# Performance work log

Hardware: AMD Instinct MI355X
Metric: run time of the kernel (lower is better)

## Reference

```python
import jax, jax.numpy as jnp
import numpy as np

B, S, V, D = 4, 128, 50257, 1024

def setup_inputs() -> dict:
    key = jax.random.key(0)
    k1, k2 = jax.random.split(key)
    # pred_probs: a probability simplex over vocab per (b, s); module initializes
    # to uniform by default, we use normalized uniform noise for a non-degenerate test.
    p = jax.random.uniform(k1, (B, S, V), dtype=jnp.float32) + 1e-3
    pred_probs = p / jnp.sum(p, axis=-1, keepdims=True)
    embed_weight = jax.random.normal(k2, (V, D), dtype=jnp.float32) * 0.02
    return {"pred_probs": pred_probs, "embed_weight": embed_weight}

def reference(pred_probs, embed_weight):
    # do_sample=False, st=False default path of TargetProbability.forward_multiple
    # predictions: argmax over vocab
    predictions = jnp.argmax(pred_probs, axis=-1)  # [B, S] int
    # soft embedding: (pred_probs.unsqueeze(-1) * embed_lut.weight).sum(-2)
    # == GEMM over the vocab dim, avoiding the [B,S,V,D] intermediate.
    pred_emb = jnp.einsum('bsv,vd->bsd', pred_probs, embed_weight)  # [B, S, D]
    return pred_emb, predictions, pred_probs
```

## Files before the change

kernel.cpp:

```cpp
#include <hip/hip_runtime.h>

#define MROWS 512
#define VDIM  50257
#define KP    50304
#define NDIM  1024
#define NST32 1572
#define KSPLIT 32
#define SC     25
#define PRED_OFF 524288
#define PP_OFF   524800
#define NPREP  4096
#define CHUNK  6288
#define NCONVW 12576

typedef unsigned short u16;
typedef unsigned int   u32;
typedef unsigned long long u64;
typedef __bf16 bf16x8 __attribute__((ext_vector_type(8)));
typedef u16    u16x8  __attribute__((ext_vector_type(8)));
typedef float  f32x4  __attribute__((ext_vector_type(4)));
typedef float  f32x4u __attribute__((ext_vector_type(4), aligned(4)));

__device__ __forceinline__ u16 f2bf(float f) {
  u32 u = __float_as_uint(f);
  u32 r = (u + 0x7fffu + ((u >> 16) & 1u)) >> 16;
  return (u16)r;
}

__device__ __forceinline__ void gl_lds16(const u16* g, u16* l) {
  __builtin_amdgcn_global_load_lds(
      (const __attribute__((address_space(1))) u32*)(g),
      (__attribute__((address_space(3))) u32*)(l), 16, 0, 0);
}

__global__ __launch_bounds__(256) void prep_fused(const float* __restrict__ P,
                                                  const float* __restrict__ W,
                                                  float* __restrict__ out,
                                                  u16* __restrict__ A,
                                                  u16* __restrict__ BT,
                                                  u64* __restrict__ amax)
{
  const int tid = threadIdx.x;
  const int bx  = blockIdx.x;
  if (bx < NPREP) {
    const int m  = bx >> 3;
    const int c  = bx & 7;
    const int s0 = c * CHUNK;
    const int len = min(VDIM - s0, CHUNK);
    const float* row = P + (size_t)m * VDIM;
    float*       crw = out + PP_OFF + (size_t)m * VDIM;
    u16*        arow = A + (size_t)m * KP;

    if (tid < 32) { f32x4 z = {}; *(f32x4*)(out + (size_t)m * NDIM + c * 128 + tid * 4) = z; }

    u64 best = 0;
#define TRK(val, idx) do { \
      u64 pk = ((u64)__float_as_uint(val) << 32) | (u64)(0xFFFFu - (u32)(idx)); \
      best = best > pk ? best : pk; } while (0)
#define GRP(cc) do {                                                     \
      f32x4u va = *(const f32x4u*)(row + (cc));                          \
      f32x4u vb = *(const f32x4u*)(row + (cc) + 4);                      \
      *(f32x4u*)(crw + (cc))     = va;                                   \
      *(f32x4u*)(crw + (cc) + 4) = vb;                                   \
      u16x8 o;                                                           \
      o[0]=f2bf(va[0]); o[1]=f2bf(va[1]); o[2]=f2bf(va[2]); o[3]=f2bf(va[3]); \
      o[4]=f2bf(vb[0]); o[5]=f2bf(vb[1]); o[6]=f2bf(vb[2]); o[7]=f2bf(vb[3]); \
      *(u16x8*)(arow + (cc)) = o;                                        \
      TRK(va[0],(cc)); TRK(va[1],(cc)+1); TRK(va[2],(cc)+2); TRK(va[3],(cc)+3); \
      TRK(vb[0],(cc)+4); TRK(vb[1],(cc)+5); TRK(vb[2],(cc)+6); TRK(vb[3],(cc)+7); \
    } while (0)

    const int ng = len >> 3;
    int i = tid;
    for (; i + 256 < ng; i += 512) {
      const int c0 = s0 + (i << 3);
      const int c1 = c0 + 2048;
      GRP(c0);
      GRP(c1);
    }
    if (i < ng) GRP(s0 + (i << 3));
    if (tid < (len & 7)) {
      const int col = s0 + (ng << 3) + tid;
      float v = row[col];
      crw[col] = v;
      arow[col] = f2bf(v);
      TRK(v, col);
    }
#undef GRP
#undef TRK
    if (c == 7 && tid < KP - VDIM) arow[VDIM + tid] = 0;

    __shared__ u64 sb[256];
    sb[tid] = best;
    __syncthreads();
    for (int s = 128; s > 0; s >>= 1) {
      if (tid < s) { u64 o = sb[tid + s]; if (o > sb[tid]) sb[tid] = o; }
      __syncthreads();
    }
    if (tid == 0) atomicMax(&amax[m], sb[0]);
  } else {
    const int cidx = bx - NPREP;
    __shared__ u16 t[64][65];
    const int dt  = cidx & 15;
    const int vt  = cidx >> 4;
    const int v0  = vt << 6;
    const int d0  = dt << 6;
    const int c16 = tid & 15;
    const int r16 = tid >> 4;
#pragma unroll
    for (int p = 0; p < 4; ++p) {
      const int v  = v0 + p * 16 + r16;
      const int vl = p * 16 + r16;
      float4 w = make_float4(0.f, 0.f, 0.f, 0.f);
      if (v < VDIM) w = *(const float4*)(W + (size_t)v * NDIM + d0 + c16 * 4);
      t[c16 * 4 + 0][vl] = f2bf(w.x);
      t[c16 * 4 + 1][vl] = f2bf(w.y);
      t[c16 * 4 + 2][vl] = f2bf(w.z);
      t[c16 * 4 + 3][vl] = f2bf(w.w);
    }
    __syncthreads();
#pragma unroll
    for (int p = 0; p < 4; ++p) {
      const int dl = p * 16 + r16;
      const int vl = c16 * 4;
      ushort4 o;
      o.x = t[dl][vl]; o.y = t[dl][vl + 1]; o.z = t[dl][vl + 2]; o.w = t[dl][vl + 3];
      *(ushort4*)(BT + (size_t)(d0 + dl) * KP + v0 + vl) = o;
    }
  }
}

__global__ __launch_bounds__(512, 1) void gemm_kernel(const u16* __restrict__ A,
                                                      const u16* __restrict__ BT,
                                                      const u64* __restrict__ amax,
                                                      float* __restrict__ out)
{
  __shared__ u16 ldsA[4][256 * 32];
  __shared__ u16 ldsB[4][256 * 32];

  const int bx  = blockIdx.x;
  const int kc  = (bx & 7) | ((bx >> 6) << 3);
  const int mn  = (bx >> 3) & 7;
  const int m0  = (mn & 1) << 8;
  const int n0  = (mn >> 1) << 8;
  const int ks0 = kc * SC * 2;
  const int ks1 = min(NST32, ks0 + SC * 2);
  const int tid  = threadIdx.x;
  const int wid  = tid >> 6;
  const int lane = tid & 63;
  const int wr   = wid >> 2;
  const int wc   = wid & 3;

  if (bx == 0) {
    u64 p = amax[tid];
    out[PRED_OFF + tid] = (float)(0xFFFF - (int)(p & 0xFFFFu));
  }

  const int sp  = lane >> 3;
  const int sx  = (lane & 7) ^ sp;
  const int srow = 2 * sp + (sx >> 2);
  const int skel = (sx & 3) << 3;
  const u16* gA = A  + (size_t)(m0 + wid * 32 + srow) * KP + skel;
  const u16* gB = BT + (size_t)(n0 + wid * 32 + srow) * KP + skel;

  f32x4 acc[8][4] = {};

  const int r   = lane & 15;
  const int q4  = lane >> 4;
  const int sl  = (((r & 1) << 2) | q4) ^ ((r >> 1) & 7);
  const int rb2A = (wr * 128 + (r & ~1)) * 32 + sl * 8;
  const int rb2B = (wc * 64  + (r & ~1)) * 32 + sl * 8;

#define STAGE_A(buf, ks) do {                                            \
    const size_t k_ = (size_t)(ks) << 5;                                 \
    gl_lds16(gA + k_,                 &ldsA[buf][(wid * 32) * 32]);      \
    gl_lds16(gA + k_ + (size_t)16*KP, &ldsA[buf][(wid * 32 + 16) * 32]); \
  } while (0)
#define STAGE_B(buf, ks) do {                                            \
    const size_t k_ = (size_t)(ks) << 5;                                 \
    gl_lds16(gB + k_,                 &ldsB[buf][(wid * 32) * 32]);      \
    gl_lds16(gB + k_ + (size_t)16*KP, &ldsB[buf][(wid * 32 + 16) * 32]); \
  } while (0)

  STAGE_A(0, ks0); STAGE_B(0, ks0);
  if (ks0 + 1 < ks1) { STAGE_A(1, ks0 + 1); STAGE_B(1, ks0 + 1); }
  if (ks0 + 2 < ks1) { STAGE_A(2, ks0 + 2); STAGE_B(2, ks0 + 2); }
  if (ks0 + 2 < ks1)      asm volatile("s_waitcnt vmcnt(8)" ::: "memory");
  else if (ks0 + 1 < ks1) asm volatile("s_waitcnt vmcnt(4)" ::: "memory");
  else                    asm volatile("s_waitcnt vmcnt(0)" ::: "memory");
  __builtin_amdgcn_s_barrier();

  int b = 0;
  for (int ks = ks0; ks < ks1; ++ks) {
    const u16* lA = ldsA[b];
    const u16* lB = ldsB[b];

    bf16x8 av[4], bv[4];
#pragma unroll
    for (int i = 0; i < 4; ++i) av[i] = *(const bf16x8*)(lA + rb2A + i * 512);
#pragma unroll
    for (int j = 0; j < 4; ++j) bv[j] = *(const bf16x8*)(lB + rb2B + j * 512);
    if (ks + 3 < ks1) STAGE_A((b + 3) & 3, ks + 3);
    __builtin_amdgcn_s_barrier();
    asm volatile("s_waitcnt lgkmcnt(0)" ::: "memory");
    __builtin_amdgcn_sched_barrier(0);
    __builtin_amdgcn_s_setprio(1);
#pragma unroll
    for (int i = 0; i < 4; ++i)
#pragma unroll
      for (int j = 0; j < 4; ++j)
        acc[i][j] = __builtin_amdgcn_mfma_f32_16x16x32_bf16(av[i], bv[j], acc[i][j], 0, 0, 0);
    __builtin_amdgcn_s_setprio(0);
    __builtin_amdgcn_s_barrier();

    bf16x8 aw[4];
#pragma unroll
    for (int i = 0; i < 4; ++i) aw[i] = *(const bf16x8*)(lA + rb2A + (i + 4) * 512);
    if (ks + 3 < ks1) STAGE_B((b + 3) & 3, ks + 3);
    __builtin_amdgcn_s_barrier();
    asm volatile("s_waitcnt lgkmcnt(0)" ::: "memory");
    __builtin_amdgcn_sched_barrier(0);
    __builtin_amdgcn_s_setprio(1);
#pragma unroll
    for (int i = 0; i < 4; ++i)
#pragma unroll
      for (int j = 0; j < 4; ++j)
        acc[i + 4][j] = __builtin_amdgcn_mfma_f32_16x16x32_bf16(aw[i], bv[j], acc[i + 4][j], 0, 0, 0);
    __builtin_amdgcn_s_setprio(0);
    if (ks + 3 < ks1)      asm volatile("s_waitcnt vmcnt(8)" ::: "memory");
    else if (ks + 2 < ks1) asm volatile("s_waitcnt vmcnt(4)" ::: "memory");
    else if (ks + 1 < ks1) asm volatile("s_waitcnt vmcnt(0)" ::: "memory");
    __builtin_amdgcn_s_barrier();
    b = (b + 1) & 3;
  }
#undef STAGE_A
#undef STAGE_B

  const int col = lane & 15;
  const int r4  = q4 << 2;
#pragma unroll
  for (int i = 0; i < 8; ++i)
#pragma unroll
    for (int j = 0; j < 4; ++j)
#pragma unroll
      for (int rr = 0; rr < 4; ++rr) {
        const int mm = m0 + wr * 128 + i * 16 + r4 + rr;
        const int nn = n0 + wc * 64 + j * 16 + col;
        atomicAdd(out + (size_t)mm * NDIM + nn, acc[i][j][rr]);
      }
}

extern "C" void kernel_launch(void* const* d_in, const int* in_sizes, int n_in,
                              void* d_out, int out_size, void* d_ws, size_t ws_size,
                              hipStream_t stream) {
  const float* P = (const float*)d_in[0];
  const float* W = (const float*)d_in[1];
  float* out = (float*)d_out;
  u64* amax = (u64*)d_ws;
  u16* A  = (u16*)((char*)d_ws + 4096);
  u16* BT = A + (size_t)MROWS * KP;

  hipMemsetAsync(amax, 0, MROWS * sizeof(u64), stream);
  prep_fused<<<NPREP + NCONVW, 256, 0, stream>>>(P, W, out, A, BT, amax);
  gemm_kernel<<<256, 512, 0, stream>>>(A, BT, amax, out);
}
```

Before: 223.6 us.

## Split prep kernel, double split-K, and switch GEMM to 2-stage double buffering

Splits the fused prep kernel into separate P-conversion/argmax and W-transpose kernels, and doubles the GEMM split-K from 32 to 64 chunks, launching 512 blocks with launch bounds allowing 2 blocks per CU. The GEMM pipeline drops from a 4-deep LDS ring with interleaved half-steps to a simpler 2-deep double buffer, which halves LDS so two workgroups can be co-resident. The intent is more parallelism and occupancy across the machine. In exchange, prefetch depth shrinks, there are twice as many atomic adds into the output, and there is one extra kernel launch.

```diff
diff --git a/kernel.cpp b/kernel.cpp
--- a/kernel.cpp
+++ b/kernel.cpp
@@ -5,8 +5,7 @@
 #define KP    50304
 #define NDIM  1024
 #define NST32 1572
-#define KSPLIT 32
-#define SC     25
+#define KSPLIT 64
 #define PRED_OFF 524288
 #define PP_OFF   524800
 #define NPREP  4096
@@ -33,118 +32,119 @@
       (__attribute__((address_space(3))) u32*)(l), 16, 0, 0);
 }
 
-__global__ __launch_bounds__(256) void prep_fused(const float* __restrict__ P,
-                                                  const float* __restrict__ W,
-                                                  float* __restrict__ out,
-                                                  u16* __restrict__ A,
-                                                  u16* __restrict__ BT,
-                                                  u64* __restrict__ amax)
+__global__ __launch_bounds__(256) void prep_kernel(const float* __restrict__ P,
+                                                   float* __restrict__ out,
+                                                   u16* __restrict__ A,
+                                                   u64* __restrict__ amax)
 {
   const int tid = threadIdx.x;
   const int bx  = blockIdx.x;
-  if (bx < NPREP) {
-    const int m  = bx >> 3;
-    const int c  = bx & 7;
-    const int s0 = c * CHUNK;
-    const int len = min(VDIM - s0, CHUNK);
-    const float* row = P + (size_t)m * VDIM;
-    float*       crw = out + PP_OFF + (size_t)m * VDIM;
-    u16*        arow = A + (size_t)m * KP;
-
-    if (tid < 32) { f32x4 z = {}; *(f32x4*)(out + (size_t)m * NDIM + c * 128 + tid * 4) = z; }
-
-    u64 best = 0;
+  const int m  = bx >> 3;
+  const int c  = bx & 7;
+  const int s0 = c * CHUNK;
+  const int len = min(VDIM - s0, CHUNK);
+  const float* row = P + (size_t)m * VDIM;
+  float*       crw = out + PP_OFF + (size_t)m * VDIM;
+  u16*        arow = A + (size_t)m * KP;
+
+  if (tid < 32) { f32x4 z = {}; *(f32x4*)(out + (size_t)m * NDIM + c * 128 + tid * 4) = z; }
+
+  u64 best = 0;
 #define TRK(val, idx) do { \
-      u64 pk = ((u64)__float_as_uint(val) << 32) | (u64)(0xFFFFu - (u32)(idx)); \
-      best = best > pk ? best : pk; } while (0)
+    u64 pk = ((u64)__float_as_uint(val) << 32) | (u64)(0xFFFFu - (u32)(idx)); \
+    best = best > pk ? best : pk; } while (0)
 #define GRP(cc) do {                                                     \
-      f32x4u va = *(const f32x4u*)(row + (cc));                          \
-      f32x4u vb = *(const f32x4u*)(row + (cc) + 4);                      \
-      *(f32x4u*)(crw + (cc))     = va;                                   \
-      *(f32x4u*)(crw + (cc) + 4) = vb;                                   \
-      u16x8 o;                                                           \
-      o[0]=f2bf(va[0]); o[1]=f2bf(va[1]); o[2]=f2bf(va[2]); o[3]=f2bf(va[3]); \
-      o[4]=f2bf(vb[0]); o[5]=f2bf(vb[1]); o[6]=f2bf(vb[2]); o[7]=f2bf(vb[3]); \
-      *(u16x8*)(arow + (cc)) = o;                                        \
-      TRK(va[0],(cc)); TRK(va[1],(cc)+1); TRK(va[2],(cc)+2); TRK(va[3],(cc)+3); \
-      TRK(vb[0],(cc)+4); TRK(vb[1],(cc)+5); TRK(vb[2],(cc)+6); TRK(vb[3],(cc)+7); \
-    } while (0)
-
-    const int ng = len >> 3;
-    int i = tid;
-    for (; i + 256 < ng; i += 512) {
-      const int c0 = s0 + (i << 3);
-      const int c1 = c0 + 2048;
-      GRP(c0);
-      GRP(c1);
-    }
-    if (i < ng) GRP(s0 + (i << 3));
-    if (tid < (len & 7)) {
-      const int col = s0 + (ng << 3) + tid;
-      float v = row[col];
-      crw[col] = v;
-      arow[col] = f2bf(v);
-      TRK(v, col);
-    }
+    f32x4u va = *(const f32x4u*)(row + (cc));                            \
+    f32x4u vb = *(const f32x4u*)(row + (cc) + 4);                        \
+    *(f32x4u*)(crw + (cc))     = va;                                     \
+    *(f32x4u*)(crw + (cc) + 4) = vb;                                     \
+    u16x8 o;                                                             \
+    o[0]=f2bf(va[0]); o[1]=f2bf(va[1]); o[2]=f2bf(va[2]); o[3]=f2bf(va[3]); \
+    o[4]=f2bf(vb[0]); o[5]=f2bf(vb[1]); o[6]=f2bf(vb[2]); o[7]=f2bf(vb[3]); \
+    *(u16x8*)(arow + (cc)) = o;                                          \
+    TRK(va[0],(cc)); TRK(va[1],(cc)+1); TRK(va[2],(cc)+2); TRK(va[3],(cc)+3); \
+    TRK(vb[0],(cc)+4); TRK(vb[1],(cc)+5); TRK(vb[2],(cc)+6); TRK(vb[3],(cc)+7); \
+  } while (0)
+
+  const int ng = len >> 3;
+  int i = tid;
+  for (; i + 256 < ng; i += 512) {
+    const int c0 = s0 + (i << 3);
+    const int c1 = c0 + 2048;
+    GRP(c0);
+    GRP(c1);
+  }
+  if (i < ng) GRP(s0 + (i << 3));
+  if (tid < (len & 7)) {
+    const int col = s0 + (ng << 3) + tid;
+    float v = row[col];
+    crw[col] = v;
+    arow[col] = f2bf(v);
+    TRK(v, col);
+  }
 #undef GRP
 #undef TRK
-    if (c == 7 && tid < KP - VDIM) arow[VDIM + tid] = 0;
-
-    __shared__ u64 sb[256];
-    sb[tid] = best;
+  if (c == 7 && tid < KP - VDIM) arow[VDIM + tid] = 0;
+
+  __shared__ u64 sb[256];
+  sb[tid] = best;
+  __syncthreads();
+  for (int s = 128; s > 0; s >>= 1) {
+    if (tid < s) { u64 o = sb[tid + s]; if (o > sb[tid]) sb[tid] = o; }
     __syncthreads();
-    for (int s = 128; s > 0; s >>= 1) {
-      if (tid < s) { u64 o = sb[tid + s]; if (o > sb[tid]) sb[tid] = o; }
-      __syncthreads();
-    }
-    if (tid == 0) atomicMax(&amax[m], sb[0]);
-  } else {
-    const int cidx = bx - NPREP;
-    __shared__ u16 t[64][65];
-    const int dt  = cidx & 15;
-    const int vt  = cidx >> 4;
-    const int v0  = vt << 6;
-    const int d0  = dt << 6;
-    const int c16 = tid & 15;
-    const int r16 = tid >> 4;
-#pragma unroll
-    for (int p = 0; p < 4; ++p) {
-      const int v  = v0 + p * 16 + r16;
-      const int vl = p * 16 + r16;
-      float4 w = make_float4(0.f, 0.f, 0.f, 0.f);
-      if (v < VDIM) w = *(const float4*)(W + (size_t)v * NDIM + d0 + c16 * 4);
-      t[c16 * 4 + 0][vl] = f2bf(w.x);
-      t[c16 * 4 + 1][vl] = f2bf(w.y);
-      t[c16 * 4 + 2][vl] = f2bf(w.z);
-      t[c16 * 4 + 3][vl] = f2bf(w.w);
-    }
-    __syncthreads();
-#pragma unroll
-    for (int p = 0; p < 4; ++p) {
-      const int dl = p * 16 + r16;
-      const int vl = c16 * 4;
-      ushort4 o;
-      o.x = t[dl][vl]; o.y = t[dl][vl + 1]; o.z = t[dl][vl + 2]; o.w = t[dl][vl + 3];
-      *(ushort4*)(BT + (size_t)(d0 + dl) * KP + v0 + vl) = o;
-    }
-  }
-}
-
-__global__ __launch_bounds__(512, 1) void gemm_kernel(const u16* __restrict__ A,
+  }
+  if (tid == 0) atomicMax(&amax[m], sb[0]);
+}
+
+__global__ __launch_bounds__(256) void convw_kernel(const float* __restrict__ W,
+                                                    u16* __restrict__ BT)
+{
+  const int cidx = blockIdx.x;
+  __shared__ u16 t[64][65];
+  const int tid = threadIdx.x;
+  const int dt  = cidx & 15;
+  const int vt  = cidx >> 4;
+  const int v0  = vt << 6;
+  const int d0  = dt << 6;
+  const int c16 = tid & 15;
+  const int r16 = tid >> 4;
+#pragma unroll
+  for (int p = 0; p < 4; ++p) {
+    const int v  = v0 + p * 16 + r16;
+    const int vl = p * 16 + r16;
+    float4 w = make_float4(0.f, 0.f, 0.f, 0.f);
+    if (v < VDIM) w = *(const float4*)(W + (size_t)v * NDIM + d0 + c16 * 4);
+    t[c16 * 4 + 0][vl] = f2bf(w.x);
+    t[c16 * 4 + 1][vl] = f2bf(w.y);
+    t[c16 * 4 + 2][vl] = f2bf(w.z);
+    t[c16 * 4 + 3][vl] = f2bf(w.w);
+  }
+  __syncthreads();
+#pragma unroll
+  for (int p = 0; p < 4; ++p) {
+    const int dl = p * 16 + r16;
+    const int vl = c16 * 4;
+    ushort4 o;
+    o.x = t[dl][vl]; o.y = t[dl][vl + 1]; o.z = t[dl][vl + 2]; o.w = t[dl][vl + 3];
+    *(ushort4*)(BT + (size_t)(d0 + dl) * KP + v0 + vl) = o;
+  }
+}
+
+__global__ __launch_bounds__(512, 2) void gemm_kernel(const u16* __restrict__ A,
                                                       const u16* __restrict__ BT,
                                                       const u64* __restrict__ amax,
                                                       float* __restrict__ out)
 {
-  __shared__ u16 ldsA[4][256 * 32];
-  __shared__ u16 ldsB[4][256 * 32];
+  __shared__ u16 ldsA[2][256 * 32];
+  __shared__ u16 ldsB[2][256 * 32];
 
   const int bx  = blockIdx.x;
   const int kc  = (bx & 7) | ((bx >> 6) << 3);
   const int mn  = (bx >> 3) & 7;
   const int m0  = (mn & 1) << 8;
   const int n0  = (mn >> 1) << 8;
-  const int ks0 = kc * SC * 2;
-  const int ks1 = min(NST32, ks0 + SC * 2);
+  const int ks0 = (kc * NST32) >> 6;
+  const int ks1 = ((kc + 1) * NST32) >> 6;
   const int tid  = threadIdx.x;
   const int wid  = tid >> 6;
   const int lane = tid & 63;
@@ -171,70 +171,44 @@
   const int rb2A = (wr * 128 + (r & ~1)) * 32 + sl * 8;
   const int rb2B = (wc * 64  + (r & ~1)) * 32 + sl * 8;
 
-#define STAGE_A(buf, ks) do {                                            \
+#define STAGE(buf, ks) do {                                              \
     const size_t k_ = (size_t)(ks) << 5;                                 \
     gl_lds16(gA + k_,                 &ldsA[buf][(wid * 32) * 32]);      \
     gl_lds16(gA + k_ + (size_t)16*KP, &ldsA[buf][(wid * 32 + 16) * 32]); \
-  } while (0)
-#define STAGE_B(buf, ks) do {                                            \
-    const size_t k_ = (size_t)(ks) << 5;                                 \
     gl_lds16(gB + k_,                 &ldsB[buf][(wid * 32) * 32]);      \
     gl_lds16(gB + k_ + (size_t)16*KP, &ldsB[buf][(wid * 32 + 16) * 32]); \
   } while (0)
 
-  STAGE_A(0, ks0); STAGE_B(0, ks0);
-  if (ks0 + 1 < ks1) { STAGE_A(1, ks0 + 1); STAGE_B(1, ks0 + 1); }
-  if (ks0 + 2 < ks1) { STAGE_A(2, ks0 + 2); STAGE_B(2, ks0 + 2); }
-  if (ks0 + 2 < ks1)      asm volatile("s_waitcnt vmcnt(8)" ::: "memory");
-  else if (ks0 + 1 < ks1) asm volatile("s_waitcnt vmcnt(4)" ::: "memory");
-  else                    asm volatile("s_waitcnt vmcnt(0)" ::: "memory");
-  __builtin_amdgcn_s_barrier();
+  STAGE(0, ks0);
+  if (ks0 + 1 < ks1) STAGE(1, ks0 + 1);
 
   int b = 0;
   for (int ks = ks0; ks < ks1; ++ks) {
+    if (ks + 1 < ks1) asm volatile("s_waitcnt vmcnt(4)" ::: "memory");
+    else              asm volatile("s_waitcnt vmcnt(0)" ::: "memory");
+    __builtin_amdgcn_s_barrier();
+
     const u16* lA = ldsA[b];
     const u16* lB = ldsB[b];
-
-    bf16x8 av[4], bv[4];
-#pragma unroll
-    for (int i = 0; i < 4; ++i) av[i] = *(const bf16x8*)(lA + rb2A + i * 512);
+    bf16x8 av[8], bv[4];
+#pragma unroll
+    for (int i = 0; i < 8; ++i) av[i] = *(const bf16x8*)(lA + rb2A + i * 512);
 #pragma unroll
     for (int j = 0; j < 4; ++j) bv[j] = *(const bf16x8*)(lB + rb2B + j * 512);
-    if (ks + 3 < ks1) STAGE_A((b + 3) & 3, ks + 3);
-    __builtin_amdgcn_s_barrier();
-    asm volatile("s_waitcnt lgkmcnt(0)" ::: "memory");
-    __builtin_amdgcn_sched_barrier(0);
+
     __builtin_amdgcn_s_setprio(1);
 #pragma unroll
-    for (int i = 0; i < 4; ++i)
+    for (int i = 0; i < 8; ++i)
 #pragma unroll
       for (int j = 0; j < 4; ++j)
         acc[i][j] = __builtin_amdgcn_mfma_f32_16x16x32_bf16(av[i], bv[j], acc[i][j], 0, 0, 0);
     __builtin_amdgcn_s_setprio(0);
+
     __builtin_amdgcn_s_barrier();
-
-    bf16x8 aw[4];
-#pragma unroll
-    for (int i = 0; i < 4; ++i) aw[i] = *(const bf16x8*)(lA + rb2A + (i + 4) * 512);
-    if (ks + 3 < ks1) STAGE_B((b + 3) & 3, ks + 3);
-    __builtin_amdgcn_s_barrier();
-    asm volatile("s_waitcnt lgkmcnt(0)" ::: "memory");
-    __builtin_amdgcn_sched_barrier(0);
-    __builtin_amdgcn_s_setprio(1);
-#pragma unroll
-    for (int i = 0; i < 4; ++i)
-#pragma unroll
-      for (int j = 0; j < 4; ++j)
-        acc[i + 4][j] = __builtin_amdgcn_mfma_f32_16x16x32_bf16(aw[i], bv[j], acc[i + 4][j], 0, 0, 0);
-    __builtin_amdgcn_s_setprio(0);
-    if (ks + 3 < ks1)      asm volatile("s_waitcnt vmcnt(8)" ::: "memory");
-    else if (ks + 2 < ks1) asm volatile("s_waitcnt vmcnt(4)" ::: "memory");
-    else if (ks + 1 < ks1) asm volatile("s_waitcnt vmcnt(0)" ::: "memory");
-    __builtin_amdgcn_s_barrier();
-    b = (b + 1) & 3;
-  }
-#undef STAGE_A
-#undef STAGE_B
+    if (ks + 2 < ks1) STAGE(b, ks + 2);
+    b ^= 1;
+  }
+#undef STAGE
 
   const int col = lane & 15;
   const int r4  = q4 << 2;
@@ -261,6 +235,7 @@
   u16* BT = A + (size_t)MROWS * KP;
 
   hipMemsetAsync(amax, 0, MROWS * sizeof(u64), stream);
-  prep_fused<<<NPREP + NCONVW, 256, 0, stream>>>(P, W, out, A, BT, amax);
-  gemm_kernel<<<256, 512, 0, stream>>>(A, BT, amax, out);
-}
+  prep_kernel<<<NPREP, 256, 0, stream>>>(P, out, A, amax);
+  convw_kernel<<<NCONVW, 256, 0, stream>>>(W, BT);
+  gemm_kernel<<<512, 512, 0, stream>>>(A, BT, amax, out);
+}
```

Result: slower. 284.0 us (+27.0%).
